# Kernel optimization log

Measured on AMD Instinct MI355X. Metric: run time of the kernel, lower is better.

## Reference

```python
import jax, jax.numpy as jnp
import numpy as np

NEG_SLOPE = 0.2


def _segment_softmax(logits, seg, num_segments):
    m = jax.ops.segment_max(logits, seg, num_segments=num_segments)
    m = jnp.where(jnp.isfinite(m), m, 0.0)
    e = jnp.exp(logits - m[seg])
    s = jax.ops.segment_sum(e, seg, num_segments=num_segments)
    return e / (s[seg] + 1e-16)


def _gat_conv(x, src, dst, W, a_src, a_dst, b, num_nodes):
    # PyG GATConv, heads=1, concat=True, add_self_loops already applied to src/dst.
    h = x @ W                                  # [N, F_out]
    alpha_src = h @ a_src                      # [N]
    alpha_dst = h @ a_dst                      # [N]
    logits = jax.nn.leaky_relu(alpha_src[src] + alpha_dst[dst], NEG_SLOPE)  # [E]
    alpha = _segment_softmax(logits, dst, num_nodes)                        # [E]
    out = jax.ops.segment_sum(alpha[:, None] * h[src], dst, num_segments=num_nodes)
    return out + b


def setup_inputs() -> dict:
    key = jax.random.key(0)
    ks = jax.random.split(key, 16)
    N, E, F_in = 50000, 1600000, 256
    x = jax.random.normal(ks[0], (N, F_in), dtype=jnp.float32)
    edge_index = jax.random.randint(ks[1], (2, E), 0, N, dtype=jnp.int64)
    edge_attr = jax.random.normal(ks[2], (E, 1), dtype=jnp.float32)

    def glorot(k, shape):
        fan = sum(shape) if len(shape) > 1 else shape[0]
        return jax.random.normal(k, shape, dtype=jnp.float32) * jnp.sqrt(2.0 / fan)

    params = {
        "W1": glorot(ks[3], (F_in, 48)), "as1": glorot(ks[4], (48,)),
        "ad1": glorot(ks[5], (48,)),     "b1": jnp.zeros((48,), jnp.float32),
        "W2": glorot(ks[6], (48, 60)),   "as2": glorot(ks[7], (60,)),
        "ad2": glorot(ks[8], (60,)),     "b2": jnp.zeros((60,), jnp.float32),
        "W3": glorot(ks[9], (60, 1)),    "as3": glorot(ks[10], (1,)),
        "ad3": glorot(ks[11], (1,)),     "b3": jnp.zeros((1,), jnp.float32),
    }
    return {"x": x, "edge_index": edge_index, "edge_attr": edge_attr, **params}


def reference(x, edge_index, edge_attr, W1, as1, ad1, b1, W2, as2, ad2, b2, W3, as3, ad3, b3):
    # edge_attr is accepted but ignored: GATConv was built without edge_dim, so no lin_edge.
    N = x.shape[0]
    loops = jnp.arange(N, dtype=edge_index.dtype)
    src = jnp.concatenate([edge_index[0], loops])  # add_self_loops=True
    dst = jnp.concatenate([edge_index[1], loops])
    h = jax.nn.relu(_gat_conv(x, src, dst, W1, as1, ad1, b1, N))
    h = jax.nn.relu(_gat_conv(h, src, dst, W2, as2, ad2, b2, N))
    h = _gat_conv(h, src, dst, W3, as3, ad3, b3, N)
    return h.reshape(-1)  # flatten -> [N]
```

## Files before the change

### kernel.cpp

```cpp
#include <hip/hip_runtime.h>
#include <cstdint>
#include <cstddef>


__device__ __forceinline__ float leaky(float v) { return v > 0.f ? v : 0.2f * v; }

__device__ __forceinline__ unsigned short f2bf(float x) {
    unsigned int u = __float_as_uint(x);
    u = (u + 0x7FFFu + ((u >> 16) & 1u)) >> 16;
    return (unsigned short)u;
}
__device__ __forceinline__ float bf2f(unsigned short b) {
    return __uint_as_float(((unsigned int)b) << 16);
}

#define BSHIFT 7
#define BCAP   5120
#define CTILE  8192


__global__ __launch_bounds__(256) void coarse_bin_kernel(
    const int* __restrict__ ei, unsigned int* __restrict__ staged,
    int* __restrict__ gcursor, int E, int K) {
    __shared__ int hist[512];
    __shared__ int rank[512];
    __shared__ int base[512];
    for (int b = threadIdx.x; b < K; b += 256) { hist[b] = 0; rank[b] = 0; }
    __syncthreads();

    int e0 = blockIdx.x * CTILE;
    int e1 = min(E, e0 + CTILE);

    for (int e = e0 + threadIdx.x; e < e1; e += 256) {
        int d = ei[E + e];
        atomicAdd(&hist[d >> BSHIFT], 1);
    }
    __syncthreads();

    for (int b = threadIdx.x; b < K; b += 256) {
        int c = hist[b];
        base[b] = c ? atomicAdd(&gcursor[b], c) : 0;
    }
    __syncthreads();

    for (int e = e0 + threadIdx.x; e < e1; e += 256) {
        int s = ei[e];
        int d = ei[E + e];
        int b = d >> BSHIFT;
        int r = atomicAdd(&rank[b], 1);
        staged[(size_t)b * BCAP + base[b] + r] =
            ((unsigned int)(d & ((1 << BSHIFT) - 1)) << 16) | (unsigned int)s;
    }
}


__global__ __launch_bounds__(512) void bucket_scan_kernel(
    const int* __restrict__ gcursor, int* __restrict__ bbase, int K) {
    __shared__ int sh[512];
    int t = threadIdx.x;
    int v = (t < K) ? gcursor[t] : 0;
    sh[t] = v;
    __syncthreads();
    for (int off = 1; off < 512; off <<= 1) {
        int a = (t >= off) ? sh[t - off] : 0;
        __syncthreads();
        sh[t] += a;
        __syncthreads();
    }
    if (t < K) bbase[t] = sh[t] - v;
}


__global__ __launch_bounds__(256) void fine_sort_kernel(
    const unsigned int* __restrict__ staged, const int* __restrict__ gcursor,
    const int* __restrict__ bbase, int* __restrict__ rowptr, int* __restrict__ csr,
    int N, int E) {
    __shared__ int cnt[128];
    __shared__ int off[128];
    __shared__ int lcsr[BCAP];
    const int b = blockIdx.x;
    const int t = threadIdx.x;
    const int c = gcursor[b];
    const int gb = bbase[b];
    const unsigned int* rec = staged + (size_t)b * BCAP;

    if (t < 128) cnt[t] = 0;
    __syncthreads();

    for (int i = t; i < c; i += 256) atomicAdd(&cnt[rec[i] >> 16], 1);
    __syncthreads();

    if (t < 128) off[t] = cnt[t];
    __syncthreads();
    for (int s = 1; s < 128; s <<= 1) {
        int a = (t >= s && t < 128) ? off[t - s] : 0;
        __syncthreads();
        if (t < 128) off[t] += a;
        __syncthreads();
    }

    if (t < 128) {
        int excl = off[t] - cnt[t];
        int n = (b << BSHIFT) + t;
        if (n <= N) rowptr[n] = gb + excl;
        cnt[t] = excl;
    }
    if (b == 0 && t == 0) rowptr[N] = E;
    __syncthreads();

    for (int i = t; i < c; i += 256) {
        unsigned int r = rec[i];
        int p = atomicAdd(&cnt[r >> 16], 1);
        lcsr[p] = (int)(r & 0xFFFFu);
    }
    __syncthreads();

    for (int i = t; i < c; i += 256) csr[gb + i] = lcsr[i];
}


template <int FIN, int FOUT, int FT, int M>
__global__ __launch_bounds__(256) void gemm_alpha_kernel(
    const float* __restrict__ X, const float* __restrict__ W,
    const float* __restrict__ avs, const float* __restrict__ avd,
    unsigned short* __restrict__ hb, float* __restrict__ asrc, float* __restrict__ adst,
    int N) {
    static_assert(4 * FT == FOUT, "FT must be FOUT/4");
    constexpr int PITCH = FIN + 4;
    __shared__ float Wt[FOUT][PITCH];
    for (int idx = threadIdx.x; idx < FOUT * FIN; idx += 256) {
        int k = idx % FIN, f = idx / FIN;
        Wt[f][k] = W[k * FOUT + f];
    }
    __syncthreads();

    const int j = threadIdx.x & 3;
    const int i = threadIdx.x >> 2;
    const int nbase = blockIdx.x * 64 * M + i * M;

    float acc[M][FT];
#pragma unroll
    for (int m = 0; m < M; m++)
#pragma unroll
        for (int c = 0; c < FT; c++) acc[m][c] = 0.f;

    const float* xrow[M];
#pragma unroll
    for (int m = 0; m < M; m++) {
        int n = nbase + m;
        if (n > N - 1) n = N - 1;
        xrow[m] = X + (size_t)n * FIN;
    }

    for (int k = 0; k < FIN; k += 4) {
        float4 xv[M];
#pragma unroll
        for (int m = 0; m < M; m++) xv[m] = *(const float4*)(xrow[m] + k);
#pragma unroll
        for (int c = 0; c < FT; c++) {
            float4 wv = *(const float4*)&Wt[j * FT + c][k];
#pragma unroll
            for (int m = 0; m < M; m++) {
                acc[m][c] = fmaf(xv[m].x, wv.x,
                             fmaf(xv[m].y, wv.y,
                              fmaf(xv[m].z, wv.z,
                               fmaf(xv[m].w, wv.w, acc[m][c]))));
            }
        }
    }

    float asv[FT], adv[FT];
#pragma unroll
    for (int c = 0; c < FT; c++) {
        asv[c] = avs[j * FT + c];
        adv[c] = avd[j * FT + c];
    }

#pragma unroll
    for (int m = 0; m < M; m++) {
        int n = nbase + m;
        float ps = 0.f, pd = 0.f;
#pragma unroll
        for (int c = 0; c < FT; c++) {
            ps = fmaf(acc[m][c], asv[c], ps);
            pd = fmaf(acc[m][c], adv[c], pd);
        }
        ps += __shfl_xor(ps, 1, 64); ps += __shfl_xor(ps, 2, 64);
        pd += __shfl_xor(pd, 1, 64); pd += __shfl_xor(pd, 2, 64);
        if (n < N) {
            if (j == 0) { asrc[n] = ps; adst[n] = pd; }
#pragma unroll
            for (int c = 0; c < FT; c++)
                hb[(size_t)n * 64 + j * FT + c] = f2bf(acc[m][c]);
        }
    }
}


#define CHUNK 128

template <int FOUT, bool RELU>
__global__ __launch_bounds__(256) void agg_bf16_kernel(
    const int* __restrict__ rowptr, const int* __restrict__ csr,
    const float* __restrict__ asrc, const float* __restrict__ adst,
    const unsigned short* __restrict__ hb, const float* __restrict__ bias,
    float* __restrict__ OUT, int N) {
    __shared__ int2 wslds[4][CHUNK];
    const int wv = threadIdx.x >> 6;
    int n = blockIdx.x * 4 + wv;
    if (n >= N) return;
    const int lane = threadIdx.x & 63;
    const int rs = rowptr[n], re = rowptr[n + 1];
    const float ad_n = adst[n];
    const float wself = __expf(leaky(asrc[n] + ad_n));
    const int fc = (lane < FOUT) ? lane : FOUT - 1;

    float acc = wself * bf2f(hb[(size_t)n * 64 + fc]);
    float wpart = 0.f;

    for (int base = rs; base < re; base += CHUNK) {
        const int cnt = min(CHUNK, re - base);
        if (lane < cnt) {
            int s = csr[base + lane];
            float w = __expf(leaky(asrc[s] + ad_n));
            wpart += w;
            wslds[wv][lane] = make_int2(s, __float_as_int(w));
        }
        int i = 0;
        for (; i + 8 <= cnt; i += 8) {
            int2 p[8];
#pragma unroll
            for (int u = 0; u < 8; u++) p[u] = wslds[wv][i + u];
            float hv[8];
#pragma unroll
            for (int u = 0; u < 8; u++) hv[u] = bf2f(hb[(size_t)p[u].x * 64 + fc]);
#pragma unroll
            for (int u = 0; u < 8; u++) acc = fmaf(__int_as_float(p[u].y), hv[u], acc);
        }
        for (; i < cnt; i++) {
            int2 pp = wslds[wv][i];
            acc = fmaf(__int_as_float(pp.y), bf2f(hb[(size_t)pp.x * 64 + fc]), acc);
        }
    }

#pragma unroll
    for (int off = 32; off; off >>= 1) wpart += __shfl_xor(wpart, off, 64);
    float ssum = wpart + wself;

    if (lane < FOUT) {
        float o = acc / (ssum + 1e-16f) + bias[lane];
        if (RELU) o = fmaxf(o, 0.f);
        OUT[(size_t)n * FOUT + lane] = o;
    }
}


__global__ __launch_bounds__(256) void gemm_out1_kernel(
    const float* __restrict__ act, const float* __restrict__ W3,
    float* __restrict__ h3, int N) {
    __shared__ float w[60];
    if (threadIdx.x < 60) w[threadIdx.x] = W3[threadIdx.x];
    __syncthreads();
    int n = blockIdx.x * 256 + threadIdx.x;
    if (n >= N) return;
    const float4* row = (const float4*)(act + (size_t)n * 60);
    float s = 0.f;
#pragma unroll
    for (int q = 0; q < 15; q++) {
        float4 v = row[q];
        s = fmaf(v.x, w[4 * q + 0],
             fmaf(v.y, w[4 * q + 1],
              fmaf(v.z, w[4 * q + 2],
               fmaf(v.w, w[4 * q + 3], s))));
    }
    h3[n] = s;
}


__global__ __launch_bounds__(256) void agg1_kernel(
    const int* __restrict__ rowptr, const int* __restrict__ csr,
    const float* __restrict__ h3,
    const float* __restrict__ as3p, const float* __restrict__ ad3p,
    const float* __restrict__ bias, float* __restrict__ OUT, int N) {
    int n = blockIdx.x * 4 + (threadIdx.x >> 6);
    if (n >= N) return;
    int lane = threadIdx.x & 63;
    int rs = rowptr[n], re = rowptr[n + 1];
    const float a_s = as3p[0];
    float hn = h3[n];
    float adn = ad3p[0] * hn;
    float wself = __expf(leaky(a_s * hn + adn));

    float ssum = 0.f, accv = 0.f;
    for (int e = rs + lane; e < re; e += 64) {
        float hs = h3[csr[e]];
        float w = __expf(leaky(a_s * hs + adn));
        ssum += w;
        accv = fmaf(w, hs, accv);
    }
#pragma unroll
    for (int off = 32; off; off >>= 1) {
        ssum += __shfl_xor(ssum, off, 64);
        accv += __shfl_xor(accv, off, 64);
    }
    ssum += wself;
    accv = fmaf(wself, hn, accv);
    if (lane == 0) OUT[n] = accv / (ssum + 1e-16f) + bias[0];
}


extern "C" void kernel_launch(void* const* d_in, const int* in_sizes, int n_in,
                              void* d_out, int out_size, void* d_ws, size_t ws_size,
                              hipStream_t stream) {
    const float* x      = (const float*)d_in[0];
    const int*   ei     = (const int*)d_in[1];
    const float* W1  = (const float*)d_in[3];
    const float* as1 = (const float*)d_in[4];
    const float* ad1 = (const float*)d_in[5];
    const float* b1  = (const float*)d_in[6];
    const float* W2  = (const float*)d_in[7];
    const float* as2 = (const float*)d_in[8];
    const float* ad2 = (const float*)d_in[9];
    const float* b2  = (const float*)d_in[10];
    const float* W3  = (const float*)d_in[11];
    const float* as3 = (const float*)d_in[12];
    const float* ad3 = (const float*)d_in[13];
    const float* b3  = (const float*)d_in[14];

    const int N = in_sizes[0] / 256;
    const int E = in_sizes[1] / 2;
    const int K = (N + (1 << BSHIFT) - 1) >> BSHIFT;

    char* p = (char*)d_ws;
    auto alloc = [&](size_t bytes) -> void* {
        void* r = (void*)p;
        p += ((bytes + 255) / 256) * 256;
        return r;
    };
    int*   gcursor = (int*)alloc(512 * 4);
    int*   bbase   = (int*)alloc(512 * 4);
    int*   rowptr  = (int*)alloc(((size_t)N + 1) * 4);
    int*   csr     = (int*)alloc((size_t)E * 4);
    unsigned short* hb = (unsigned short*)alloc((size_t)N * 64 * 2);
    float* actbuf  = (float*)alloc((size_t)N * 60 * 4);
    float* h3      = (float*)alloc((size_t)N * 4);
    float* asrc    = (float*)alloc((size_t)N * 4);
    float* adst    = (float*)alloc((size_t)N * 4);
    unsigned int* staged = (unsigned int*)actbuf;

    hipMemsetAsync(gcursor, 0, 512 * 4, stream);
    int cblocks = (E + CTILE - 1) / CTILE;
    coarse_bin_kernel<<<cblocks, 256, 0, stream>>>(ei, staged, gcursor, E, K);
    bucket_scan_kernel<<<1, 512, 0, stream>>>(gcursor, bbase, K);
    fine_sort_kernel<<<K, 256, 0, stream>>>(staged, gcursor, bbase, rowptr, csr, N, E);

    int gblocks = (N + 127) / 128;
    int ablocks = (N + 3) / 4;

    gemm_alpha_kernel<256, 48, 12, 2><<<gblocks, 256, 0, stream>>>(x, W1, as1, ad1, hb, asrc, adst, N);
    agg_bf16_kernel<48, true><<<ablocks, 256, 0, stream>>>(rowptr, csr, asrc, adst, hb, b1, actbuf, N);

    gemm_alpha_kernel<48, 60, 15, 2><<<gblocks, 256, 0, stream>>>(actbuf, W2, as2, ad2, hb, asrc, adst, N);
    agg_bf16_kernel<60, true><<<ablocks, 256, 0, stream>>>(rowptr, csr, asrc, adst, hb, b2, actbuf, N);

    gemm_out1_kernel<<<(N + 255) / 256, 256, 0, stream>>>(actbuf, W3, h3, N);
    agg1_kernel<<<ablocks, 256, 0, stream>>>(rowptr, csr, h3, as3, ad3, b3, (float*)d_out, N);
}
```

Measured before the change: 298.4 us.

## Split GEMM output features across blocks and fuse layer-3 projection into aggregation

The feature GEMM now splits the output columns over a second grid dimension (2 slices for layer 1, 3 for layer 2), so more blocks run with a smaller shared weight tile. The per-node attention scalars are built from partial sums with atomicAdd, which needs memsets before each GEMM. Layer-2 aggregation is fused with the 60→1 projection through a wave reduction, so the separate projection kernel goes away along with the write and re-read of the 60-wide activation buffer. The price is duplicated reads of X across feature slices, extra atomics and memset launches, and float atomic ordering that can change results slightly.

```diff
diff --git a/kernel.cpp b/kernel.cpp
--- a/kernel.cpp
+++ b/kernel.cpp
@@ -119,18 +119,20 @@
 }
 
 
-template <int FIN, int FOUT, int FT, int M>
+template <int FIN, int FOUT, int FSUB, int M>
 __global__ __launch_bounds__(256) void gemm_alpha_kernel(
     const float* __restrict__ X, const float* __restrict__ W,
     const float* __restrict__ avs, const float* __restrict__ avd,
     unsigned short* __restrict__ hb, float* __restrict__ asrc, float* __restrict__ adst,
     int N) {
-    static_assert(4 * FT == FOUT, "FT must be FOUT/4");
+    constexpr int FT = FSUB / 4;
+    static_assert(4 * FT == FSUB, "FSUB must be divisible by 4");
     constexpr int PITCH = FIN + 4;
-    __shared__ float Wt[FOUT][PITCH];
-    for (int idx = threadIdx.x; idx < FOUT * FIN; idx += 256) {
+    __shared__ float Wt[FSUB][PITCH];
+    const int fbase = blockIdx.y * FSUB;
+    for (int idx = threadIdx.x; idx < FSUB * FIN; idx += 256) {
         int k = idx % FIN, f = idx / FIN;
-        Wt[f][k] = W[k * FOUT + f];
+        Wt[f][k] = W[k * FOUT + fbase + f];
     }
     __syncthreads();
 
@@ -172,8 +174,8 @@
     float asv[FT], adv[FT];
 #pragma unroll
     for (int c = 0; c < FT; c++) {
-        asv[c] = avs[j * FT + c];
-        adv[c] = avd[j * FT + c];
+        asv[c] = avs[fbase + j * FT + c];
+        adv[c] = avd[fbase + j * FT + c];
     }
 
 #pragma unroll
@@ -188,10 +190,13 @@
         ps += __shfl_xor(ps, 1, 64); ps += __shfl_xor(ps, 2, 64);
         pd += __shfl_xor(pd, 1, 64); pd += __shfl_xor(pd, 2, 64);
         if (n < N) {
-            if (j == 0) { asrc[n] = ps; adst[n] = pd; }
+            if (j == 0) {
+                atomicAdd(&asrc[n], ps);
+                atomicAdd(&adst[n], pd);
+            }
 #pragma unroll
             for (int c = 0; c < FT; c++)
-                hb[(size_t)n * 64 + j * FT + c] = f2bf(acc[m][c]);
+                hb[(size_t)n * 64 + fbase + j * FT + c] = f2bf(acc[m][c]);
         }
     }
 }
@@ -255,25 +260,62 @@
 }
 
 
-__global__ __launch_bounds__(256) void gemm_out1_kernel(
-    const float* __restrict__ act, const float* __restrict__ W3,
-    float* __restrict__ h3, int N) {
-    __shared__ float w[60];
-    if (threadIdx.x < 60) w[threadIdx.x] = W3[threadIdx.x];
-    __syncthreads();
-    int n = blockIdx.x * 256 + threadIdx.x;
+__global__ __launch_bounds__(256) void agg_bf16_h3_kernel(
+    const int* __restrict__ rowptr, const int* __restrict__ csr,
+    const float* __restrict__ asrc, const float* __restrict__ adst,
+    const unsigned short* __restrict__ hb, const float* __restrict__ bias,
+    const float* __restrict__ W3, float* __restrict__ h3, int N) {
+    constexpr int FOUT = 60;
+    __shared__ int2 wslds[4][CHUNK];
+    const int wv = threadIdx.x >> 6;
+    int n = blockIdx.x * 4 + wv;
     if (n >= N) return;
-    const float4* row = (const float4*)(act + (size_t)n * 60);
-    float s = 0.f;
-#pragma unroll
-    for (int q = 0; q < 15; q++) {
-        float4 v = row[q];
-        s = fmaf(v.x, w[4 * q + 0],
-             fmaf(v.y, w[4 * q + 1],
-              fmaf(v.z, w[4 * q + 2],
-               fmaf(v.w, w[4 * q + 3], s))));
-    }
-    h3[n] = s;
+    const int lane = threadIdx.x & 63;
+    const int rs = rowptr[n], re = rowptr[n + 1];
+    const float ad_n = adst[n];
+    const float wself = __expf(leaky(asrc[n] + ad_n));
+    const int fc = (lane < FOUT) ? lane : FOUT - 1;
+
+    float acc = wself * bf2f(hb[(size_t)n * 64 + fc]);
+    float wpart = 0.f;
+
+    for (int base = rs; base < re; base += CHUNK) {
+        const int cnt = min(CHUNK, re - base);
+        if (lane < cnt) {
+            int s = csr[base + lane];
+            float w = __expf(leaky(asrc[s] + ad_n));
+            wpart += w;
+            wslds[wv][lane] = make_int2(s, __float_as_int(w));
+        }
+        int i = 0;
+        for (; i + 8 <= cnt; i += 8) {
+            int2 p[8];
+#pragma unroll
+            for (int u = 0; u < 8; u++) p[u] = wslds[wv][i + u];
+            float hv[8];
+#pragma unroll
+            for (int u = 0; u < 8; u++) hv[u] = bf2f(hb[(size_t)p[u].x * 64 + fc]);
+#pragma unroll
+            for (int u = 0; u < 8; u++) acc = fmaf(__int_as_float(p[u].y), hv[u], acc);
+        }
+        for (; i < cnt; i++) {
+            int2 pp = wslds[wv][i];
+            acc = fmaf(__int_as_float(pp.y), bf2f(hb[(size_t)pp.x * 64 + fc]), acc);
+        }
+    }
+
+#pragma unroll
+    for (int off = 32; off; off >>= 1) wpart += __shfl_xor(wpart, off, 64);
+    float ssum = wpart + wself;
+
+    float t = 0.f;
+    if (lane < FOUT) {
+        float o = fmaxf(acc / (ssum + 1e-16f) + bias[lane], 0.f);
+        t = o * W3[lane];
+    }
+#pragma unroll
+    for (int off = 32; off; off >>= 1) t += __shfl_xor(t, off, 64);
+    if (lane == 0) h3[n] = t;
 }
 
 
@@ -342,7 +384,7 @@
     int*   rowptr  = (int*)alloc(((size_t)N + 1) * 4);
     int*   csr     = (int*)alloc((size_t)E * 4);
     unsigned short* hb = (unsigned short*)alloc((size_t)N * 64 * 2);
-    float* actbuf  = (float*)alloc((size_t)N * 60 * 4);
+    float* actbuf  = (float*)alloc((size_t)N * 48 * 4);
     float* h3      = (float*)alloc((size_t)N * 4);
     float* asrc    = (float*)alloc((size_t)N * 4);
     float* adst    = (float*)alloc((size_t)N * 4);
@@ -357,12 +399,17 @@
     int gblocks = (N + 127) / 128;
     int ablocks = (N + 3) / 4;
 
-    gemm_alpha_kernel<256, 48, 12, 2><<<gblocks, 256, 0, stream>>>(x, W1, as1, ad1, hb, asrc, adst, N);
+    hipMemsetAsync(asrc, 0, (size_t)N * 4, stream);
+    hipMemsetAsync(adst, 0, (size_t)N * 4, stream);
+    gemm_alpha_kernel<256, 48, 24, 2><<<dim3(gblocks, 2), 256, 0, stream>>>(
+        x, W1, as1, ad1, hb, asrc, adst, N);
     agg_bf16_kernel<48, true><<<ablocks, 256, 0, stream>>>(rowptr, csr, asrc, adst, hb, b1, actbuf, N);
 
-    gemm_alpha_kernel<48, 60, 15, 2><<<gblocks, 256, 0, stream>>>(actbuf, W2, as2, ad2, hb, asrc, adst, N);
-    agg_bf16_kernel<60, true><<<ablocks, 256, 0, stream>>>(rowptr, csr, asrc, adst, hb, b2, actbuf, N);
-
-    gemm_out1_kernel<<<(N + 255) / 256, 256, 0, stream>>>(actbuf, W3, h3, N);
+    hipMemsetAsync(asrc, 0, (size_t)N * 4, stream);
+    hipMemsetAsync(adst, 0, (size_t)N * 4, stream);
+    gemm_alpha_kernel<48, 60, 20, 2><<<dim3(gblocks, 3), 256, 0, stream>>>(
+        actbuf, W2, as2, ad2, hb, asrc, adst, N);
+    agg_bf16_h3_kernel<<<ablocks, 256, 0, stream>>>(rowptr, csr, asrc, adst, hb, b2, W3, h3, N);
+
     agg1_kernel<<<ablocks, 256, 0, stream>>>(rowptr, csr, h3, as3, ad3, b3, (float*)d_out, N);
 }
```

After: 311.6 us. 4.4% more time.
